# Kernel optimization log

Hardware: AMD Instinct MI355X
Metric: run time of the kernel (lower is better)

## Reference

```python
import jax, jax.numpy as jnp
import numpy as np

B, S, H, NH = 4, 1024, 4096, 32
QL, KVL, RD, ND, VD = 1536, 512, 64, 128, 128  # q_lora, kv_lora, rope, nope, v head dims
QHD = ND + RD  # 192
EPS = 1e-6


def setup_inputs() -> dict:
    key = jax.random.key(0)
    ks = jax.random.split(key, 10)
    def w(k, fan_in, fan_out):
        return jax.random.normal(k, (fan_in, fan_out), jnp.float32) * (fan_in ** -0.5)
    return {
        "hidden_states": jax.random.normal(ks[0], (B, S, H), jnp.float32),
        "cos": jax.random.uniform(ks[1], (S, RD), jnp.float32),
        "sin": jax.random.uniform(ks[2], (S, RD), jnp.float32),
        "position_ids": jax.random.randint(ks[3], (B, S), 0, S, jnp.int64 if jax.config.jax_enable_x64 else jnp.int32),
        "Wqa": w(ks[4], H, QL),
        "gqa": jnp.ones((QL,), jnp.float32),
        "bqa": jnp.zeros((QL,), jnp.float32),
        "Wqb": w(ks[5], QL, NH * QHD),
        "Wkva": w(ks[6], H, KVL + RD),
        "gkva": jnp.ones((KVL,), jnp.float32),
        "bkva": jnp.zeros((KVL,), jnp.float32),
        "Wkvb": w(ks[7], KVL, NH * (ND + VD)),
        "Wo": w(ks[8], NH * VD, H),
    }


def _ln(x, g, b):
    m = jnp.mean(x, -1, keepdims=True)
    v = jnp.mean(jnp.square(x - m), -1, keepdims=True)
    return (x - m) * jax.lax.rsqrt(v + EPS) * g + b


def _rotate_half(x):
    x1, x2 = jnp.split(x, 2, axis=-1)
    return jnp.concatenate([-x2, x1], axis=-1)


def _rope(t, cos_g, sin_g):
    # t: (B,S,h,RD); cos_g/sin_g: (B,S,1,RD)
    return t * cos_g + _rotate_half(t) * sin_g


def reference(hidden_states, cos, sin, position_ids, Wqa, gqa, bqa, Wqb, Wkva, gkva, bkva, Wkvb, Wo):
    hs = hidden_states
    # low-rank Q path: q_a_proj -> LN -> q_b_proj
    q = _ln(hs @ Wqa, gqa, bqa) @ Wqb                      # (B,S,NH*QHD)
    q = q.reshape(B, S, NH, QHD)
    q_nope, q_pe = q[..., :ND], q[..., ND:]                # (B,S,NH,128/64)
    # compressed KV + MQA rope key
    ckv = hs @ Wkva                                        # (B,S,KVL+RD)
    kv_c, k_pe = ckv[..., :KVL], ckv[..., KVL:]
    kv_cn = _ln(kv_c, gkva, bkva)                          # (B,S,512)
    # partial-dim RoPE on rope slices only
    cos_g = cos[position_ids][:, :, None, :]               # (B,S,1,RD)
    sin_g = sin[position_ids][:, :, None, :]
    q_pe = _rope(q_pe, cos_g, sin_g)                       # (B,S,NH,RD)
    k_pe = _rope(k_pe[:, :, None, :], cos_g, sin_g)        # (B,S,1,RD)
    # decompress latent into per-head k_nope and v
    kv = (kv_cn @ Wkvb).reshape(B, S, NH, ND + VD)
    k_nope, v = kv[..., :ND], kv[..., ND:]
    k = jnp.concatenate([k_nope, jnp.broadcast_to(k_pe, (B, S, NH, RD))], axis=-1)  # (B,S,NH,192)
    qs = jnp.concatenate([q_nope, q_pe], axis=-1)          # (B,S,NH,192)
    # causal attention
    scores = jnp.einsum('bqhd,bkhd->bhqk', qs, k) * (QHD ** -0.5)
    causal = jnp.tril(jnp.ones((S, S), bool))
    scores = jnp.where(causal, scores, jnp.finfo(scores.dtype).min)
    p = jax.nn.softmax(scores, axis=-1)                    # (B,NH,S,S)
    o = jnp.einsum('bhqk,bkhd->bqhd', p, v).reshape(B, S, NH * VD)
    return o @ Wo                                          # (B,S,H)
```

## Files before the change

kernel.cpp:

```cpp
#include <hip/hip_runtime.h>

#define B_ 4
#define S_ 1024
#define H_ 4096
#define NH_ 32
#define QHD_ 192
#define EPS_ 1e-6f

typedef __bf16 bf16x8 __attribute__((ext_vector_type(8)));
typedef float floatx4 __attribute__((ext_vector_type(4)));

__device__ __forceinline__ unsigned short f2bf(float f) {
  unsigned int u = __builtin_bit_cast(unsigned int, f);
  u += 0x7fffu + ((u >> 16) & 1u);
  return (unsigned short)(u >> 16);
}
__device__ __forceinline__ float bf2f(unsigned short s) {
  return __builtin_bit_cast(float, ((unsigned int)s) << 16);
}

__device__ __forceinline__ void gload16(const unsigned short* g, unsigned short* l) {
  __builtin_amdgcn_global_load_lds(
      (const __attribute__((address_space(1))) void*)g,
      (__attribute__((address_space(3))) void*)l, 16, 0, 0);
}

__global__ __launch_bounds__(256) void convert_kernel(
    const float* __restrict__ x, unsigned short* __restrict__ y)
{
  const int i = (blockIdx.x * 256 + threadIdx.x) * 8;
  const float4 a = *(const float4*)(x + i);
  const float4 b = *(const float4*)(x + i + 4);
  ushort4 u, v;
  u.x = f2bf(a.x); u.y = f2bf(a.y); u.z = f2bf(a.z); u.w = f2bf(a.w);
  v.x = f2bf(b.x); v.y = f2bf(b.y); v.z = f2bf(b.z); v.w = f2bf(b.w);
  *(ushort4*)(y + i) = u;
  *(ushort4*)(y + i + 4) = v;
}

__global__ __launch_bounds__(256) void transpose_kernel(
    const float* __restrict__ W, unsigned short* __restrict__ Wt,
    const int K, const int N)
{
  __shared__ float tile[32][33];
  const int tx = threadIdx.x & 31, ty = threadIdx.x >> 5;
  const int nb = blockIdx.x << 5, kb = blockIdx.y << 5;
#pragma unroll
  for (int j = 0; j < 4; ++j)
    tile[ty + j * 8][tx] = W[(size_t)(kb + ty + j * 8) * N + nb + tx];
  __syncthreads();
#pragma unroll
  for (int j = 0; j < 4; ++j)
    Wt[(size_t)(nb + ty + j * 8) * K + kb + tx] = f2bf(tile[tx][ty + j * 8]);
}

template<int OMODE>
__global__ __launch_bounds__(256, 2) void gemm_bt(
    const unsigned short* __restrict__ A, const unsigned short* __restrict__ Bt,
    void* __restrict__ Cv, const int N, const int K,
    const int lda, const int ldb, const int ldc)
{
  __shared__ unsigned short As[128 * 32];
  __shared__ unsigned short Bs[128 * 32];

  const int t = threadIdx.x;
  const int m0 = blockIdx.x * 128, n0 = blockIdx.y * 128;
  const int w = t >> 6, lane = t & 63;
  const int wm = (w >> 1) << 6, wn = (w & 1) << 6;
  const int lm = lane & 15, lq = lane >> 4;

  const floatx4 vzero = {0.f, 0.f, 0.f, 0.f};
  floatx4 acc[4][4];
#pragma unroll
  for (int i = 0; i < 4; ++i)
#pragma unroll
    for (int j = 0; j < 4; ++j) acc[i][j] = vzero;

  const int srow = (w << 5) + (lane >> 2);
  const int skc = (lane & 3) << 3;
  const unsigned short* gA = A + (size_t)(m0 + srow) * lda + skc;
  const unsigned short* gB = Bt + (size_t)(n0 + srow) * ldb + skc;
  unsigned short* lA0 = &As[(w << 1) * 512];
  unsigned short* lA1 = &As[((w << 1) + 1) * 512];
  unsigned short* lB0 = &Bs[(w << 1) * 512];
  unsigned short* lB1 = &Bs[((w << 1) + 1) * 512];

  const int nk = K >> 5;
  for (int kb = 0; kb < nk; ++kb) {
    const int k0 = kb << 5;
    __syncthreads();
    gload16(gA + k0, lA0);
    gload16(gA + (size_t)16 * lda + k0, lA1);
    gload16(gB + k0, lB0);
    gload16(gB + (size_t)16 * ldb + k0, lB1);
    __syncthreads();

    bf16x8 af[4], bfr[4];
#pragma unroll
    for (int mi = 0; mi < 4; ++mi)
      af[mi] = *(const bf16x8*)&As[(wm + mi * 16 + lm) * 32 + (lq << 3)];
#pragma unroll
    for (int ni = 0; ni < 4; ++ni)
      bfr[ni] = *(const bf16x8*)&Bs[(wn + ni * 16 + lm) * 32 + (lq << 3)];
#pragma unroll
    for (int mi = 0; mi < 4; ++mi)
#pragma unroll
      for (int ni = 0; ni < 4; ++ni)
        acc[mi][ni] = __builtin_amdgcn_mfma_f32_16x16x32_bf16(af[mi], bfr[ni], acc[mi][ni], 0, 0, 0);
  }

#pragma unroll
  for (int mi = 0; mi < 4; ++mi) {
    const int row = m0 + wm + mi * 16 + (lq << 2);
#pragma unroll
    for (int ni = 0; ni < 4; ++ni) {
      const int col = n0 + wn + ni * 16 + lm;
      if (col < N) {
#pragma unroll
        for (int r = 0; r < 4; ++r) {
          if constexpr (OMODE == 0)
            ((float*)Cv)[(size_t)(row + r) * ldc + col] = acc[mi][ni][r];
          else if constexpr (OMODE == 1)
            ((unsigned short*)Cv)[(size_t)(row + r) * ldc + col] = f2bf(acc[mi][ni][r]);
          else {
            const int rr2 = row + r;
            ((unsigned short*)Cv)[(((size_t)(rr2 >> 10) * NH_ + (col >> 8)) * S_ + (rr2 & 1023)) * 256 + (col & 255)] = f2bf(acc[mi][ni][r]);
          }
        }
      }
    }
  }
}

__global__ __launch_bounds__(256) void ln_kernel(
    const float* __restrict__ x, const float* __restrict__ g,
    const float* __restrict__ bias, unsigned short* __restrict__ y,
    const int L, const int xstride, const int ystride)
{
  __shared__ float sh[4];
  const int t = threadIdx.x;
  const float* xr = x + (size_t)blockIdx.x * xstride;
  unsigned short* yr = y + (size_t)blockIdx.x * ystride;
  const int n = L >> 8;
  float vals[6];
  float s = 0.f;
  for (int i = 0; i < n; ++i) { vals[i] = xr[t + (i << 8)]; s += vals[i]; }
#pragma unroll
  for (int off = 32; off; off >>= 1) s += __shfl_down(s, off);
  if ((t & 63) == 0) sh[t >> 6] = s;
  __syncthreads();
  const float mean = (sh[0] + sh[1] + sh[2] + sh[3]) / (float)L;
  float vs = 0.f;
  for (int i = 0; i < n; ++i) { const float d = vals[i] - mean; vs += d * d; }
#pragma unroll
  for (int off = 32; off; off >>= 1) vs += __shfl_down(vs, off);
  __syncthreads();
  if ((t & 63) == 0) sh[t >> 6] = vs;
  __syncthreads();
  const float inv = rsqrtf((sh[0] + sh[1] + sh[2] + sh[3]) / (float)L + EPS_);
  for (int i = 0; i < n; ++i) {
    const int c = t + (i << 8);
    yr[c] = f2bf((vals[i] - mean) * inv * g[c] + bias[c]);
  }
}

__global__ __launch_bounds__(256) void rope_q_kernel(
    unsigned short* __restrict__ q, const float* __restrict__ cosp,
    const float* __restrict__ sinp, const int* __restrict__ pos)
{
  const int i = blockIdx.x * 256 + threadIdx.x;
  const int p = i & 31;
  const int h = (i >> 5) & 31;
  const int bs = i >> 10;
  const int pid = pos[bs];
  const size_t base = ((size_t)bs * NH_ + h) * QHD_ + 128;
  const float x1 = bf2f(q[base + p]);
  const float x2 = bf2f(q[base + p + 32]);
  const float* cr = cosp + (size_t)pid * 64;
  const float* sr = sinp + (size_t)pid * 64;
  q[base + p]      = f2bf(x1 * cr[p] - x2 * sr[p]);
  q[base + p + 32] = f2bf(x2 * cr[p + 32] + x1 * sr[p + 32]);
}

__global__ __launch_bounds__(256) void rope_k_kernel(
    const float* __restrict__ ckv, const float* __restrict__ cosp,
    const float* __restrict__ sinp, const int* __restrict__ pos,
    unsigned short* __restrict__ kpe)
{
  const int i = blockIdx.x * 256 + threadIdx.x;
  const int p = i & 31;
  const int bs = i >> 5;
  const int pid = pos[bs];
  const float* row = ckv + (size_t)bs * 576 + 512;
  const float x1 = row[p], x2 = row[p + 32];
  const float* cr = cosp + (size_t)pid * 64;
  const float* sr = sinp + (size_t)pid * 64;
  kpe[(size_t)bs * 64 + p]      = f2bf(x1 * cr[p] - x2 * sr[p]);
  kpe[(size_t)bs * 64 + p + 32] = f2bf(x2 * cr[p + 32] + x1 * sr[p + 32]);
}

__global__ __launch_bounds__(512, 4) void attn_kernel(
    const unsigned short* __restrict__ qb, const unsigned short* __restrict__ kvb,
    const unsigned short* __restrict__ kpe, unsigned short* __restrict__ o)
{
  __shared__ unsigned short Ks[64 * 200];
  __shared__ unsigned short Vt[128 * 72];
  __shared__ unsigned short Ps[8 * 16 * 72];

  const int t = threadIdx.x;
  const int q0 = (int)gridDim.x - 1 - (int)blockIdx.x;
  const int h = blockIdx.y, b = blockIdx.z;
  const int w = t >> 6, lane = t & 63;
  const int lm = lane & 15, lq = lane >> 4;
  const float SCALE2 = 0.10411754645f;

  const unsigned short* qp = qb + (((size_t)b * S_ + (q0 << 7) + (w << 4) + lm) * NH_ + h) * QHD_;
  bf16x8 qf[6];
#pragma unroll
  for (int s = 0; s < 6; ++s) qf[s] = *(const bf16x8*)(qp + s * 32 + (lq << 3));

  const floatx4 vzero = {0.f, 0.f, 0.f, 0.f};
  floatx4 of[8];
#pragma unroll
  for (int i = 0; i < 8; ++i) of[i] = vzero;
  float mrow[4] = {-1e30f, -1e30f, -1e30f, -1e30f};
  float lrow[4] = {0.f, 0.f, 0.f, 0.f};

  const unsigned short* kvbase = kvb + (size_t)(b * NH_ + h) * S_ * 256;
  const unsigned short* kpbase = kpe + (size_t)b * S_ * 64;

  uint4 rKa0, rKa1, rKp0, rVa0, rVb0;

  const int tK  = (t >> 4) * 256 + ((t & 15) << 3);
  const int tKp = (t >> 3) * 64 + ((t & 7) << 3);
  const int cg  = t & 15;
  const int kp  = t >> 4;
  const int tV  = (kp << 1) * 256 + 128 + (cg << 3);

#define LOAD_TILE(KT) do { \
    const unsigned short* kvt_ = kvbase + (size_t)((KT) << 6) * 256; \
    const unsigned short* kpt_ = kpbase + (size_t)((KT) << 6) * 64;  \
    rKa0 = *(const uint4*)(kvt_ + tK);                                \
    rKa1 = *(const uint4*)(kvt_ + 32 * 256 + tK);                     \
    rKp0 = *(const uint4*)(kpt_ + tKp);                               \
    rVa0 = *(const uint4*)(kvt_ + tV);                                \
    rVb0 = *(const uint4*)(kvt_ + tV + 256);                          \
  } while (0)

  LOAD_TILE(0);

  const int wKs  = (t >> 4) * 200 + ((t & 15) << 3);
  const int wKps = (t >> 3) * 200 + 128 + ((t & 7) << 3);
  const int scv  = (kp ^ ((cg & 7) << 2)) << 1;
  unsigned short* vbp = &Vt[(cg << 3) * 72 + scv];

  const int ktmax = (q0 << 1) + 1;
  const int qrel0 = (q0 << 7) + (w << 4);

  for (int kt = 0; kt <= ktmax; ++kt) {
    __syncthreads();
    *(uint4*)&Ks[wKs]            = rKa0;
    *(uint4*)&Ks[32 * 200 + wKs] = rKa1;
    *(uint4*)&Ks[wKps]           = rKp0;
    *(unsigned int*)(vbp + 0 * 72) = (rVa0.x & 0xffffu) | (rVb0.x << 16);
    *(unsigned int*)(vbp + 1 * 72) = (rVa0.x >> 16)     | (rVb0.x & 0xffff0000u);
    *(unsigned int*)(vbp + 2 * 72) = (rVa0.y & 0xffffu) | (rVb0.y << 16);
    *(unsigned int*)(vbp + 3 * 72) = (rVa0.y >> 16)     | (rVb0.y & 0xffff0000u);
    *(unsigned int*)(vbp + 4 * 72) = (rVa0.z & 0xffffu) | (rVb0.z << 16);
    *(unsigned int*)(vbp + 5 * 72) = (rVa0.z >> 16)     | (rVb0.z & 0xffff0000u);
    *(unsigned int*)(vbp + 6 * 72) = (rVa0.w & 0xffffu) | (rVb0.w << 16);
    *(unsigned int*)(vbp + 7 * 72) = (rVa0.w >> 16)     | (rVb0.w & 0xffff0000u);
    __syncthreads();
    if (kt < ktmax) LOAD_TILE(kt + 1);

    const int rel = qrel0 - (kt << 6);
    if (rel >= 0) {
      const int nimax = (rel >= 64) ? 3 : (rel >> 4);

      floatx4 s0v = vzero, s1v = vzero, s2v = vzero, s3v = vzero;
#define QKNI(SACC, NI) do { \
      _Pragma("unroll") \
      for (int s = 0; s < 6; ++s) { \
        const bf16x8 kf = *(const bf16x8*)&Ks[((NI) * 16 + lm) * 200 + s * 32 + (lq << 3)]; \
        SACC = __builtin_amdgcn_mfma_f32_16x16x32_bf16(qf[s], kf, SACC, 0, 0, 0); \
      } } while (0)
      QKNI(s0v, 0);
      if (nimax >= 1) QKNI(s1v, 1);
      if (nimax >= 2) QKNI(s2v, 2);
      if (nimax >= 3) QKNI(s3v, 3);
#undef QKNI

      const bool dg = (rel < 64);
#pragma unroll
      for (int r = 0; r < 4; ++r) {
        const int rq = (lq << 2) + r;
        float a0 = s0v[r] * SCALE2;
        float a1 = s1v[r] * SCALE2;
        float a2 = s2v[r] * SCALE2;
        float a3 = s3v[r] * SCALE2;
        if (nimax < 1) a1 = -1e30f;
        if (nimax < 2) a2 = -1e30f;
        if (nimax < 3) a3 = -1e30f;
        if (dg) {
          const bool m = lm > rq;
          if (nimax == 0 && m) a0 = -1e30f;
          if (nimax == 1 && m) a1 = -1e30f;
          if (nimax == 2 && m) a2 = -1e30f;
          if (nimax == 3 && m) a3 = -1e30f;
        }
        float mx = fmaxf(fmaxf(a0, a1), fmaxf(a2, a3));
#pragma unroll
        for (int off = 8; off; off >>= 1) mx = fmaxf(mx, __shfl_xor(mx, off));
        const float mnew = fmaxf(mrow[r], mx);
        const float al = __builtin_amdgcn_exp2f(mrow[r] - mnew);
        mrow[r] = mnew;
        const float p0 = __builtin_amdgcn_exp2f(a0 - mnew);
        const float p1 = __builtin_amdgcn_exp2f(a1 - mnew);
        const float p2 = __builtin_amdgcn_exp2f(a2 - mnew);
        const float p3 = __builtin_amdgcn_exp2f(a3 - mnew);
        unsigned short* pr = &Ps[(w * 16 + rq) * 72 + lm];
        pr[0]  = f2bf(p0);
        pr[16] = f2bf(p1);
        pr[32] = f2bf(p2);
        pr[48] = f2bf(p3);
        float ps = (p0 + p1) + (p2 + p3);
#pragma unroll
        for (int off = 8; off; off >>= 1) ps += __shfl_xor(ps, off);
        lrow[r] = lrow[r] * al + ps;
#pragma unroll
        for (int vt = 0; vt < 8; ++vt) of[vt][r] *= al;
      }

      {
        const bf16x8 pf = *(const bf16x8*)&Ps[(w * 16 + lm) * 72 + (lq << 3)];
#pragma unroll
        for (int vt = 0; vt < 8; ++vt) {
          const int rr = vt * 16 + lm;
          const int c0 = (lq << 2);
          const bf16x8 vf = *(const bf16x8*)&Vt[rr * 72 + ((c0 ^ (((rr >> 3) & 7) << 2)) << 1)];
          of[vt] = __builtin_amdgcn_mfma_f32_16x16x32_bf16(pf, vf, of[vt], 0, 0, 0);
        }
      }
      if (rel >= 32) {
        const bf16x8 pf = *(const bf16x8*)&Ps[(w * 16 + lm) * 72 + 32 + (lq << 3)];
#pragma unroll
        for (int vt = 0; vt < 8; ++vt) {
          const int rr = vt * 16 + lm;
          const int c0 = 16 + (lq << 2);
          const bf16x8 vf = *(const bf16x8*)&Vt[rr * 72 + ((c0 ^ (((rr >> 3) & 7) << 2)) << 1)];
          of[vt] = __builtin_amdgcn_mfma_f32_16x16x32_bf16(pf, vf, of[vt], 0, 0, 0);
        }
      }
    }
  }

#pragma unroll
  for (int r = 0; r < 4; ++r) {
    const int qrow = (q0 << 7) + (w << 4) + (lq << 2) + r;
    const float inv = 1.f / lrow[r];
    unsigned short* orow = o + ((size_t)b * S_ + qrow) * 4096 + h * 128;
#pragma unroll
    for (int vt = 0; vt < 8; ++vt)
      orow[vt * 16 + lm] = f2bf(of[vt][r] * inv);
  }
#undef LOAD_TILE
}

extern "C" void kernel_launch(void* const* d_in, const int* in_sizes, int n_in,
                              void* d_out, int out_size, void* d_ws, size_t ws_size,
                              hipStream_t stream) {
  (void)in_sizes; (void)n_in; (void)out_size; (void)ws_size;
  const float* hs   = (const float*)d_in[0];
  const float* cosp = (const float*)d_in[1];
  const float* sinp = (const float*)d_in[2];
  const int*   pos  = (const int*)d_in[3];
  const float* Wqa  = (const float*)d_in[4];
  const float* gqa  = (const float*)d_in[5];
  const float* bqa  = (const float*)d_in[6];
  const float* Wqb  = (const float*)d_in[7];
  const float* Wkva = (const float*)d_in[8];
  const float* gkva = (const float*)d_in[9];
  const float* bkva = (const float*)d_in[10];
  const float* Wkvb = (const float*)d_in[11];
  const float* Wo   = (const float*)d_in[12];
  float* out = (float*)d_out;

  char* ws = (char*)d_ws;
  unsigned short* hsb   = (unsigned short*)(ws);
  float*          q_a   = (float*)(ws + 33554432);
  unsigned short* qb    = (unsigned short*)(ws);
  unsigned short* WqaT  = (unsigned short*)(ws + 58720256);
  unsigned short* WkvaT = (unsigned short*)(ws + 71303168);
  unsigned short* qln   = (unsigned short*)(ws + 58720256);
  unsigned short* kvln  = (unsigned short*)(ws + 71303168);
  unsigned short* WqbT  = (unsigned short*)(ws + 76546048);
  float*          ckv   = (float*)(ws + 95420416);
  unsigned short* WkvbT = (unsigned short*)(ws + 104857600);
  unsigned short* ob    = (unsigned short*)(ws + 76546048);
  unsigned short* WoT   = (unsigned short*)(ws + 113246208);
  unsigned short* kvb   = (unsigned short*)(ws + 146800640);
  unsigned short* kpe   = (unsigned short*)(ws + 213909504);

  const dim3 blk(256);
  convert_kernel<<<dim3(8192), blk, 0, stream>>>(hs, hsb);
  transpose_kernel<<<dim3(48, 128), blk, 0, stream>>>(Wqa, WqaT, 4096, 1536);
  transpose_kernel<<<dim3(18, 128), blk, 0, stream>>>(Wkva, WkvaT, 4096, 576);
  transpose_kernel<<<dim3(192, 48), blk, 0, stream>>>(Wqb, WqbT, 1536, 6144);
  transpose_kernel<<<dim3(256, 16), blk, 0, stream>>>(Wkvb, WkvbT, 512, 8192);
  transpose_kernel<<<dim3(128, 128), blk, 0, stream>>>(Wo, WoT, 4096, 4096);

  gemm_bt<0><<<dim3(32, 12), blk, 0, stream>>>(hsb, WqaT, q_a, 1536, 4096, 4096, 4096, 1536);
  gemm_bt<0><<<dim3(32, 5), blk, 0, stream>>>(hsb, WkvaT, ckv, 576, 4096, 4096, 4096, 576);
  ln_kernel<<<dim3(4096), blk, 0, stream>>>(q_a, gqa, bqa, qln, 1536, 1536, 1536);
  ln_kernel<<<dim3(4096), blk, 0, stream>>>(ckv, gkva, bkva, kvln, 512, 576, 512);
  rope_k_kernel<<<dim3(512), blk, 0, stream>>>(ckv, cosp, sinp, pos, kpe);
  gemm_bt<1><<<dim3(32, 48), blk, 0, stream>>>(qln, WqbT, qb, 6144, 1536, 1536, 1536, 6144);
  rope_q_kernel<<<dim3(16384), blk, 0, stream>>>(qb, cosp, sinp, pos);
  gemm_bt<2><<<dim3(32, 64), blk, 0, stream>>>(kvln, WkvbT, kvb, 8192, 512, 512, 512, 8192);
  attn_kernel<<<dim3(8, 32, 4), dim3(512), 0, stream>>>(qb, kvb, kpe, ob);
  gemm_bt<0><<<dim3(32, 32), blk, 0, stream>>>(ob, WoT, out, 4096, 4096, 4096, 4096, 4096);
}
```

Measured before the change: 983.3 us.

## Fuse q_a/kv_a GEMMs, use DPP reductions and lazy softmax rescale in attention

```diff
diff --git a/kernel.cpp b/kernel.cpp
--- a/kernel.cpp
+++ b/kernel.cpp
@@ -23,6 +23,26 @@
   __builtin_amdgcn_global_load_lds(
       (const __attribute__((address_space(1))) void*)g,
       (__attribute__((address_space(3))) void*)l, 16, 0, 0);
+}
+
+template<int C>
+__device__ __forceinline__ float dpp_ror(float v) {
+  return __builtin_bit_cast(float,
+      __builtin_amdgcn_mov_dpp(__builtin_bit_cast(int, v), 0x120 | C, 0xf, 0xf, false));
+}
+__device__ __forceinline__ float rmax16(float v) {
+  v = fmaxf(v, dpp_ror<1>(v));
+  v = fmaxf(v, dpp_ror<2>(v));
+  v = fmaxf(v, dpp_ror<4>(v));
+  v = fmaxf(v, dpp_ror<8>(v));
+  return v;
+}
+__device__ __forceinline__ float rsum16(float v) {
+  v += dpp_ror<1>(v);
+  v += dpp_ror<2>(v);
+  v += dpp_ror<4>(v);
+  v += dpp_ror<8>(v);
+  return v;
 }
 
 __global__ __launch_bounds__(256) void convert_kernel(
@@ -57,7 +77,7 @@
 template<int OMODE>
 __global__ __launch_bounds__(256, 2) void gemm_bt(
     const unsigned short* __restrict__ A, const unsigned short* __restrict__ Bt,
-    void* __restrict__ Cv, const int N, const int K,
+    void* __restrict__ Cv, void* __restrict__ Cv2, const int N, const int K,
     const int lda, const int ldb, const int ldc)
 {
   __shared__ unsigned short As[128 * 32];
@@ -122,9 +142,14 @@
             ((float*)Cv)[(size_t)(row + r) * ldc + col] = acc[mi][ni][r];
           else if constexpr (OMODE == 1)
             ((unsigned short*)Cv)[(size_t)(row + r) * ldc + col] = f2bf(acc[mi][ni][r]);
-          else {
+          else if constexpr (OMODE == 2) {
             const int rr2 = row + r;
             ((unsigned short*)Cv)[(((size_t)(rr2 >> 10) * NH_ + (col >> 8)) * S_ + (rr2 & 1023)) * 256 + (col & 255)] = f2bf(acc[mi][ni][r]);
+          } else {
+            if (col < 1536)
+              ((float*)Cv)[(size_t)(row + r) * 1536 + col] = acc[mi][ni][r];
+            else
+              ((float*)Cv2)[(size_t)(row + r) * 576 + (col - 1536)] = acc[mi][ni][r];
           }
         }
       }
@@ -205,7 +230,7 @@
 {
   __shared__ unsigned short Ks[64 * 200];
   __shared__ unsigned short Vt[128 * 72];
-  __shared__ unsigned short Ps[8 * 16 * 72];
+  __shared__ unsigned short Ps[8 * 16 * 68];
 
   const int t = threadIdx.x;
   const int q0 = (int)gridDim.x - 1 - (int)blockIdx.x;
@@ -278,6 +303,7 @@
       const int nimax = (rel >= 64) ? 3 : (rel >> 4);
 
       floatx4 s0v = vzero, s1v = vzero, s2v = vzero, s3v = vzero;
+      __builtin_amdgcn_s_setprio(1);
 #define QKNI(SACC, NI) do { \
       _Pragma("unroll") \
       for (int s = 0; s < 6; ++s) { \
@@ -289,6 +315,7 @@
       if (nimax >= 2) QKNI(s2v, 2);
       if (nimax >= 3) QKNI(s3v, 3);
 #undef QKNI
+      __builtin_amdgcn_s_setprio(0);
 
       const bool dg = (rel < 64);
 #pragma unroll
@@ -309,30 +336,32 @@
           if (nimax == 3 && m) a3 = -1e30f;
         }
         float mx = fmaxf(fmaxf(a0, a1), fmaxf(a2, a3));
-#pragma unroll
-        for (int off = 8; off; off >>= 1) mx = fmaxf(mx, __shfl_xor(mx, off));
-        const float mnew = fmaxf(mrow[r], mx);
-        const float al = __builtin_amdgcn_exp2f(mrow[r] - mnew);
-        mrow[r] = mnew;
-        const float p0 = __builtin_amdgcn_exp2f(a0 - mnew);
-        const float p1 = __builtin_amdgcn_exp2f(a1 - mnew);
-        const float p2 = __builtin_amdgcn_exp2f(a2 - mnew);
-        const float p3 = __builtin_amdgcn_exp2f(a3 - mnew);
-        unsigned short* pr = &Ps[(w * 16 + rq) * 72 + lm];
+        mx = rmax16(mx);
+        if (!__all(mx <= mrow[r] + 6.0f)) {
+          const float mnew = fmaxf(mrow[r], mx);
+          const float al = __builtin_amdgcn_exp2f(mrow[r] - mnew);
+          mrow[r] = mnew;
+          lrow[r] *= al;
+#pragma unroll
+          for (int vt = 0; vt < 8; ++vt) of[vt][r] *= al;
+        }
+        const float p0 = __builtin_amdgcn_exp2f(a0 - mrow[r]);
+        const float p1 = __builtin_amdgcn_exp2f(a1 - mrow[r]);
+        const float p2 = __builtin_amdgcn_exp2f(a2 - mrow[r]);
+        const float p3 = __builtin_amdgcn_exp2f(a3 - mrow[r]);
+        unsigned short* pr = &Ps[(w * 16 + rq) * 68 + lm];
         pr[0]  = f2bf(p0);
         pr[16] = f2bf(p1);
         pr[32] = f2bf(p2);
         pr[48] = f2bf(p3);
         float ps = (p0 + p1) + (p2 + p3);
-#pragma unroll
-        for (int off = 8; off; off >>= 1) ps += __shfl_xor(ps, off);
-        lrow[r] = lrow[r] * al + ps;
-#pragma unroll
-        for (int vt = 0; vt < 8; ++vt) of[vt][r] *= al;
+        ps = rsum16(ps);
+        lrow[r] += ps;
       }
 
+      __builtin_amdgcn_s_setprio(1);
       {
-        const bf16x8 pf = *(const bf16x8*)&Ps[(w * 16 + lm) * 72 + (lq << 3)];
+        const bf16x8 pf = *(const bf16x8*)&Ps[(w * 16 + lm) * 68 + (lq << 3)];
 #pragma unroll
         for (int vt = 0; vt < 8; ++vt) {
           const int rr = vt * 16 + lm;
@@ -342,7 +371,7 @@
         }
       }
       if (rel >= 32) {
-        const bf16x8 pf = *(const bf16x8*)&Ps[(w * 16 + lm) * 72 + 32 + (lq << 3)];
+        const bf16x8 pf = *(const bf16x8*)&Ps[(w * 16 + lm) * 68 + 32 + (lq << 3)];
 #pragma unroll
         for (int vt = 0; vt < 8; ++vt) {
           const int rr = vt * 16 + lm;
@@ -351,6 +380,7 @@
           of[vt] = __builtin_amdgcn_mfma_f32_16x16x32_bf16(pf, vf, of[vt], 0, 0, 0);
         }
       }
+      __builtin_amdgcn_s_setprio(0);
     }
   }
 
@@ -409,14 +439,13 @@
   transpose_kernel<<<dim3(256, 16), blk, 0, stream>>>(Wkvb, WkvbT, 512, 8192);
   transpose_kernel<<<dim3(128, 128), blk, 0, stream>>>(Wo, WoT, 4096, 4096);
 
-  gemm_bt<0><<<dim3(32, 12), blk, 0, stream>>>(hsb, WqaT, q_a, 1536, 4096, 4096, 4096, 1536);
-  gemm_bt<0><<<dim3(32, 5), blk, 0, stream>>>(hsb, WkvaT, ckv, 576, 4096, 4096, 4096, 576);
+  gemm_bt<3><<<dim3(32, 17), blk, 0, stream>>>(hsb, WqaT, q_a, ckv, 2112, 4096, 4096, 4096, 0);
   ln_kernel<<<dim3(4096), blk, 0, stream>>>(q_a, gqa, bqa, qln, 1536, 1536, 1536);
   ln_kernel<<<dim3(4096), blk, 0, stream>>>(ckv, gkva, bkva, kvln, 512, 576, 512);
   rope_k_kernel<<<dim3(512), blk, 0, stream>>>(ckv, cosp, sinp, pos, kpe);
-  gemm_bt<1><<<dim3(32, 48), blk, 0, stream>>>(qln, WqbT, qb, 6144, 1536, 1536, 1536, 6144);
+  gemm_bt<1><<<dim3(32, 48), blk, 0, stream>>>(qln, WqbT, qb, nullptr, 6144, 1536, 1536, 1536, 6144);
   rope_q_kernel<<<dim3(16384), blk, 0, stream>>>(qb, cosp, sinp, pos);
-  gemm_bt<2><<<dim3(32, 64), blk, 0, stream>>>(kvln, WkvbT, kvb, 8192, 512, 512, 512, 8192);
+  gemm_bt<2><<<dim3(32, 64), blk, 0, stream>>>(kvln, WkvbT, kvb, nullptr, 8192, 512, 512, 512, 8192);
   attn_kernel<<<dim3(8, 32, 4), dim3(512), 0, stream>>>(qb, kvb, kpe, ob);
-  gemm_bt<0><<<dim3(32, 32), blk, 0, stream>>>(ob, WoT, out, 4096, 4096, 4096, 4096, 4096);
-}
+  gemm_bt<0><<<dim3(32, 32), blk, 0, stream>>>(ob, WoT, out, nullptr, 4096, 4096, 4096, 4096, 4096);
+}
```

After: 1.392 ms. 1.42x slower.
